# Kernel optimization log

Hardware: AMD Instinct MI355X
Metric: run time of the kernel (lower is better)

## Reference

```python
import jax, jax.numpy as jnp
import numpy as np

B, N, K, F = 1, 50000, 16, 128
EPS = 1e-5

def _bn(h, gamma, beta):
    # BatchNorm1d in training mode: per-feature-channel stats over (batch, nodes)
    mean = jnp.mean(h, axis=(0, 1), keepdims=True)
    var = jnp.var(h, axis=(0, 1), keepdims=True)
    return (h - mean) * jax.lax.rsqrt(var + EPS) * gamma + beta

def _rgcn(h, neighbors, W, b):
    # pad one zero node row, gather K neighbors per node, flatten, linear
    h_pad = jnp.pad(h, ((0, 0), (0, 1), (0, 0)))           # [B, N+1, F]
    gathered = h_pad[:, neighbors]                          # [B, N, K, F]
    flat = gathered.reshape(h.shape[0], neighbors.shape[0], -1)  # [B, N, K*F]
    return jnp.einsum('bnk,ok->bno', flat, W) + b

def setup_inputs():
    key = jax.random.key(0)
    ks = jax.random.split(key, 10)
    x = jax.random.normal(ks[0], (B, N, F), jnp.float32)
    graph = jax.random.randint(ks[1], (N, K, 2), 0, N)
    gamma1 = 1.0 + 0.1 * jax.random.normal(ks[2], (F,), jnp.float32)
    beta1 = 0.1 * jax.random.normal(ks[3], (F,), jnp.float32)
    gamma2 = 1.0 + 0.1 * jax.random.normal(ks[4], (F,), jnp.float32)
    beta2 = 0.1 * jax.random.normal(ks[5], (F,), jnp.float32)
    s = 1.0 / np.sqrt(K * F)
    W1 = jax.random.uniform(ks[6], (F, K * F), jnp.float32, -s, s)
    b1 = jax.random.uniform(ks[7], (F,), jnp.float32, -s, s)
    W2 = jax.random.uniform(ks[8], (F, K * F), jnp.float32, -s, s)
    b2 = jax.random.uniform(ks[9], (F,), jnp.float32, -s, s)
    return {"x": x, "graph": graph, "gamma1": gamma1, "beta1": beta1,
            "W1": W1, "b1": b1, "gamma2": gamma2, "beta2": beta2,
            "W2": W2, "b2": b2}

def reference(x, graph, gamma1, beta1, W1, b1, gamma2, beta2, W2, b2):
    neighbors = graph[..., 1]                               # [N, K]
    out = jax.nn.gelu(_bn(x, gamma1, beta1), approximate=False)
    out = _rgcn(out, neighbors, W1, b1)                     # [B, N, F]
    out = jax.nn.gelu(_bn(out, gamma2, beta2), approximate=False)
    out = _rgcn(out, neighbors, W2, b2)                     # [B, N, F]
    return out + x
```

## Files before the change

kernel.cpp:

```cpp
#include <hip/hip_runtime.h>


#define NN  50000
#define NB  500
#define NPB 100

typedef __bf16 v8bf __attribute__((ext_vector_type(8)));
typedef unsigned short u8s __attribute__((ext_vector_type(8)));
typedef float  v4f  __attribute__((ext_vector_type(4)));

__device__ __forceinline__ unsigned short f2bf(float f) {
  unsigned int u = __builtin_bit_cast(unsigned int, f);
  u += 0x7FFFu + ((u >> 16) & 1u);
  return (unsigned short)(u >> 16);
}
__device__ __forceinline__ float bf2f(unsigned short s) {
  unsigned int u = ((unsigned int)s) << 16;
  return __builtin_bit_cast(float, u);
}
__device__ __forceinline__ float gelu_f(float y) {
  return 0.5f * y * (1.0f + erff(y * 0.70710678118654752f));
}

__global__ void wconv_kernel(const float* __restrict__ W1, const float* __restrict__ W2,
                             unsigned short* __restrict__ Wt1, unsigned short* __restrict__ Wt2) {
  int t = blockIdx.x * 256 + threadIdx.x;
  const float* W = (t >= 32768) ? W2 : W1;
  unsigned short* Wt = (t >= 32768) ? Wt2 : Wt1;
  int r = t & 32767;
  int frag = r >> 6, lane = r & 63;
  int k4 = frag >> 3, c = frag & 7;
  int o  = c * 16 + (lane & 15);
  int kd = k4 * 32 + (lane >> 4) * 8;
  const float* src = W + o * 2048 + kd;
  unsigned short* dst = Wt + r * 8;
#pragma unroll
  for (int j = 0; j < 8; ++j) dst[j] = f2bf(src[j]);
}

__global__ void bn_stats_kernel(const float* __restrict__ x, float* __restrict__ part) {
  float s0=0,s1=0,s2=0,s3=0,q0=0,q1=0,q2=0,q3=0;
  for (int cb = blockIdx.x; cb < (NN*128/1024); cb += 256) {
    float4 v = reinterpret_cast<const float4*>(x)[cb * 256 + threadIdx.x];
    s0+=v.x; q0+=v.x*v.x; s1+=v.y; q1+=v.y*v.y;
    s2+=v.z; q2+=v.z*v.z; s3+=v.w; q3+=v.w*v.w;
  }
  __shared__ float ls[1024], lsq[1024];
  int fb = (threadIdx.x & 31) * 4;
  int sl = threadIdx.x >> 5;
  ls[sl*128+fb]   = s0; ls[sl*128+fb+1]  = s1; ls[sl*128+fb+2]  = s2; ls[sl*128+fb+3]  = s3;
  lsq[sl*128+fb]  = q0; lsq[sl*128+fb+1] = q1; lsq[sl*128+fb+2] = q2; lsq[sl*128+fb+3] = q3;
  __syncthreads();
  if (threadIdx.x < 128) {
    float S=0,Q=0;
#pragma unroll
    for (int s2i=0; s2i<8; ++s2i){ S += ls[s2i*128+threadIdx.x]; Q += lsq[s2i*128+threadIdx.x]; }
    part[blockIdx.x*256 + threadIdx.x]       = S;
    part[blockIdx.x*256 + 128 + threadIdx.x] = Q;
  }
}

__global__ __launch_bounds__(1024) void bn_reduce_kernel(
    const float* __restrict__ part, int nb,
    const float* __restrict__ gamma, const float* __restrict__ beta,
    float* __restrict__ scsh) {
  int f = threadIdx.x & 127;
  int g = threadIdx.x >> 7;
  float S = 0.f, Q = 0.f;
  for (int b = g; b < nb; b += 8) {
    S += part[b * 256 + f];
    Q += part[b * 256 + 128 + f];
  }
  __shared__ float ls[8][128], lq[8][128];
  ls[g][f] = S; lq[g][f] = Q;
  __syncthreads();
  if (threadIdx.x < 128) {
    float St = 0.f, Qt = 0.f;
#pragma unroll
    for (int i = 0; i < 8; ++i) { St += ls[i][f]; Qt += lq[i][f]; }
    float inv  = 1.0f / (float)NN;
    float mean = St * inv;
    float var  = fmaxf(Qt * inv - mean * mean, 0.0f);
    float sc   = gamma[f] * rsqrtf(var + 1e-5f);
    scsh[f]       = sc;
    scsh[128 + f] = beta[f] - mean * sc;
  }
}

__global__ void apply1_kernel(const float* __restrict__ x, const float* __restrict__ scsh,
                              unsigned short* __restrict__ h1) {
  int stride = gridDim.x * blockDim.x;
  for (int c = blockIdx.x * blockDim.x + threadIdx.x; c < NN*128/4; c += stride) {
    float4 v = reinterpret_cast<const float4*>(x)[c];
    int f = (c * 4) & 127;
    ushort4 o;
    o.x = f2bf(gelu_f(v.x * scsh[f]   + scsh[128+f]));
    o.y = f2bf(gelu_f(v.y * scsh[f+1] + scsh[128+f+1]));
    o.z = f2bf(gelu_f(v.z * scsh[f+2] + scsh[128+f+2]));
    o.w = f2bf(gelu_f(v.w * scsh[f+3] + scsh[128+f+3]));
    reinterpret_cast<ushort4*>(h1)[c] = o;
  }
}

template<int MODE>
__global__ __launch_bounds__(256, 2) void rgcn_kernel(
    const unsigned short* __restrict__ hb,
    const unsigned short* __restrict__ Wt,
    const int* __restrict__ graph,
    const float* __restrict__ scsh,
    const float* __restrict__ bias,
    const float* __restrict__ xres,
    float* __restrict__ outf,
    unsigned short* __restrict__ outb,
    float* __restrict__ part)
{
  __shared__ unsigned short bsm[16384];
  __shared__ float2 scp[128];

  const int tid  = threadIdx.x;
  const int wv   = tid >> 6;
  const int lane = tid & 63;
  const int l15  = lane & 15;
  const int lq   = lane >> 4;
  const int nb0  = blockIdx.x * NPB;
  const int nend = nb0 + NPB;

  if (MODE == 1 && tid < 128) scp[tid] = make_float2(scsh[tid], scsh[128 + tid]);

  v4f acc[2][8];
#pragma unroll
  for (int rf = 0; rf < 2; ++rf)
#pragma unroll
    for (int c = 0; c < 8; ++c) acc[rf][c] = (v4f){0.f, 0.f, 0.f, 0.f};

  const int an0 = min(nb0 + wv * 32 + l15,      nend - 1);
  const int an1 = min(nb0 + wv * 32 + 16 + l15, nend - 1);

  int idx0[16], idx1[16];
  {
    const int4* g0 = reinterpret_cast<const int4*>(graph + an0 * 32);
    const int4* g1 = reinterpret_cast<const int4*>(graph + an1 * 32);
#pragma unroll
    for (int j = 0; j < 8; ++j) {
      int4 t0 = g0[j], t1v = g1[j];
      idx0[2*j]   = min(max(t0.y,  0), NN - 1) * 128;
      idx0[2*j+1] = min(max(t0.w,  0), NN - 1) * 128;
      idx1[2*j]   = min(max(t1v.y, 0), NN - 1) * 128;
      idx1[2*j+1] = min(max(t1v.w, 0), NN - 1) * 128;
    }
  }

  u8s R0[2][4], R1[2][4];
#define LOADA(buf_, s_) {                                             \
    const unsigned short* r0 = hb + idx0[s_] + lq * 8;                \
    const unsigned short* r1 = hb + idx1[s_] + lq * 8;                \
    _Pragma("unroll")                                                 \
    for (int w4 = 0; w4 < 4; ++w4) {                                  \
      R0[buf_][w4] = *reinterpret_cast<const u8s*>(r0 + w4 * 32);     \
      R1[buf_][w4] = *reinterpret_cast<const u8s*>(r1 + w4 * 32);     \
    }                                                                 \
  }

#define STAGE(s_) {                                                           \
    const unsigned short* gsrc = Wt + (s_) * 16384 + wv * 4096 + lane * 8;    \
    unsigned short* ldst = &bsm[wv * 4096];                                   \
    _Pragma("unroll")                                                         \
    for (int i = 0; i < 8; ++i) {                                             \
      __builtin_amdgcn_global_load_lds(                                       \
        (const __attribute__((address_space(1))) void*)(gsrc + i * 512),      \
        (__attribute__((address_space(3))) void*)(ldst + i * 512),            \
        16, 0, 0);                                                            \
    }                                                                         \
  }

#define SLOT(s_) {                                                            \
    if ((s_) < 15) LOADA(((s_) + 1) & 1, (s_) + 1)                            \
    __builtin_amdgcn_sched_barrier(0);                                        \
    __builtin_amdgcn_s_setprio(1);                                            \
    {                                                                         \
      const int cur_ = (s_) & 1;                                              \
      _Pragma("unroll")                                                       \
      for (int w4 = 0; w4 < 4; ++w4) {                                        \
        v8bf a0v, a1v;                                                        \
        if constexpr (MODE == 0) {                                            \
          a0v = __builtin_bit_cast(v8bf, R0[cur_][w4]);                       \
          a1v = __builtin_bit_cast(v8bf, R1[cur_][w4]);                       \
        } else {                                                              \
          _Pragma("unroll")                                                   \
          for (int j = 0; j < 8; ++j) {                                       \
            float2 ss = scp[w4 * 32 + lq * 8 + j];                            \
            float t0 = bf2f(R0[cur_][w4][j]) * ss.x + ss.y;                   \
            float t1 = bf2f(R1[cur_][w4][j]) * ss.x + ss.y;                   \
            a0v[j] = (__bf16)(t0 * __builtin_amdgcn_rcpf(                     \
                         1.0f + __expf(-1.702f * t0)));                       \
            a1v[j] = (__bf16)(t1 * __builtin_amdgcn_rcpf(                     \
                         1.0f + __expf(-1.702f * t1)));                       \
          }                                                                   \
        }                                                                     \
        _Pragma("unroll")                                                     \
        for (int c = 0; c < 8; ++c) {                                         \
          v8bf b = *reinterpret_cast<const v8bf*>(                            \
              &bsm[(w4 * 8 + c) * 512 + lane * 8]);                           \
          acc[0][c] = __builtin_amdgcn_mfma_f32_16x16x32_bf16(                \
                        a0v, b, acc[0][c], 0, 0, 0);                          \
          acc[1][c] = __builtin_amdgcn_mfma_f32_16x16x32_bf16(                \
                        a1v, b, acc[1][c], 0, 0, 0);                          \
        }                                                                     \
      }                                                                       \
    }                                                                         \
    __builtin_amdgcn_s_setprio(0);                                            \
    __builtin_amdgcn_sched_barrier(0);                                        \
    __builtin_amdgcn_s_barrier();             \
    __builtin_amdgcn_sched_barrier(0);                                        \
    if ((s_) < 15) STAGE((s_) + 1)                                            \
    __syncthreads();                      \
  }

  STAGE(0)
  LOADA(0, 0)
  __syncthreads();

  SLOT(0)  SLOT(1)  SLOT(2)  SLOT(3)
  SLOT(4)  SLOT(5)  SLOT(6)  SLOT(7)
  SLOT(8)  SLOT(9)  SLOT(10) SLOT(11)
  SLOT(12) SLOT(13) SLOT(14) SLOT(15)
#undef SLOT
#undef LOADA
#undef STAGE

  if constexpr (MODE == 0) {
    float* lds_s = reinterpret_cast<float*>(bsm);
    float* lds_q = lds_s + 512;
#pragma unroll
    for (int c = 0; c < 8; ++c) {
      float s = 0.f, q = 0.f;
#pragma unroll
      for (int rf = 0; rf < 2; ++rf) {
#pragma unroll
        for (int j = 0; j < 4; ++j) {
          int node = nb0 + wv * 32 + rf * 16 + lq * 4 + j;
          float v  = acc[rf][c][j];
          if (node < nend) {
            s += v; q += v * v;
            outb[node * 128 + c * 16 + l15] = f2bf(v);
          }
        }
      }
      s += __shfl_xor(s, 16, 64); s += __shfl_xor(s, 32, 64);
      q += __shfl_xor(q, 16, 64); q += __shfl_xor(q, 32, 64);
      if (lq == 0) { lds_s[wv * 128 + c * 16 + l15] = s; lds_q[wv * 128 + c * 16 + l15] = q; }
    }
    __syncthreads();
    if (tid < 128) {
      float S = lds_s[tid] + lds_s[128 + tid] + lds_s[256 + tid] + lds_s[384 + tid];
      float Q = lds_q[tid] + lds_q[128 + tid] + lds_q[256 + tid] + lds_q[384 + tid];
      part[blockIdx.x * 256 + tid]       = S;
      part[blockIdx.x * 256 + 128 + tid] = Q;
    }
  } else {
#pragma unroll
    for (int c = 0; c < 8; ++c) {
      float bv = bias[c * 16 + l15];
#pragma unroll
      for (int rf = 0; rf < 2; ++rf) {
#pragma unroll
        for (int j = 0; j < 4; ++j) {
          int node = nb0 + wv * 32 + rf * 16 + lq * 4 + j;
          if (node < nend) {
            int idx = node * 128 + c * 16 + l15;
            outf[idx] = acc[rf][c][j] + bv + xres[idx];
          }
        }
      }
    }
  }
}

extern "C" void kernel_launch(void* const* d_in, const int* in_sizes, int n_in,
                              void* d_out, int out_size, void* d_ws, size_t ws_size,
                              hipStream_t stream) {
  const float* x      = (const float*)d_in[0];
  const int*   graph  = (const int*)d_in[1];
  const float* gamma1 = (const float*)d_in[2];
  const float* beta1  = (const float*)d_in[3];
  const float* W1     = (const float*)d_in[4];
  const float* gamma2 = (const float*)d_in[6];
  const float* beta2  = (const float*)d_in[7];
  const float* W2     = (const float*)d_in[8];
  const float* b2     = (const float*)d_in[9];
  float* out = (float*)d_out;

  char* ws = (char*)d_ws;
  unsigned short* h1  = (unsigned short*)(ws);
  unsigned short* t1  = (unsigned short*)(ws + 12800000);
  unsigned short* Wt1 = (unsigned short*)(ws + 25600000);
  unsigned short* Wt2 = (unsigned short*)(ws + 26124288);
  float* p1    = (float*)(ws + 26648576);
  float* p2    = (float*)(ws + 26910720);
  float* scsh1 = (float*)(ws + 27422720);
  float* scsh2 = (float*)(ws + 27423744);

  wconv_kernel<<<256, 256, 0, stream>>>(W1, W2, Wt1, Wt2);
  bn_stats_kernel<<<256, 256, 0, stream>>>(x, p1);
  bn_reduce_kernel<<<1, 1024, 0, stream>>>(p1, 256, gamma1, beta1, scsh1);
  apply1_kernel<<<2048, 256, 0, stream>>>(x, scsh1, h1);
  rgcn_kernel<0><<<NB, 256, 0, stream>>>(h1, Wt1, graph, nullptr, nullptr, nullptr,
                                         nullptr, t1, p2);
  bn_reduce_kernel<<<1, 1024, 0, stream>>>(p2, NB, gamma2, beta2, scsh2);
  rgcn_kernel<1><<<NB, 256, 0, stream>>>(t1, Wt2, graph, scsh2, b2, x,
                                         out, nullptr, nullptr);
}
```

Measured before the change: 201.2 us.

## Precompute BN2+GELU in a separate pass and coalesce t1 stores via LDS

The second BN+GELU used to be computed inside the rgcn gather loop, so every node row was recomputed once per neighbor, 16 times in total. It now runs once per element in a new elementwise apply2 kernel, and rgcn feeds the gathered bf16 rows straight into MFMA. The second-layer GELU also changes from the sigmoid approximation to the exact erf form. The first rgcn pass now stages its bf16 output tile in LDS and writes it out with coalesced 16-byte stores. The cost is an extra launch plus one more read and write pass over a 12.8 MB buffer.

```diff
diff --git a/kernel.cpp b/kernel.cpp
--- a/kernel.cpp
+++ b/kernel.cpp
@@ -102,12 +102,26 @@
   }
 }
 
+__global__ void apply2_kernel(const unsigned short* __restrict__ t1, const float* __restrict__ scsh,
+                              unsigned short* __restrict__ h2) {
+  int stride = gridDim.x * blockDim.x;
+  for (int c = blockIdx.x * blockDim.x + threadIdx.x; c < NN*128/4; c += stride) {
+    ushort4 v = reinterpret_cast<const ushort4*>(t1)[c];
+    int f = (c * 4) & 127;
+    ushort4 o;
+    o.x = f2bf(gelu_f(bf2f(v.x) * scsh[f]   + scsh[128+f]));
+    o.y = f2bf(gelu_f(bf2f(v.y) * scsh[f+1] + scsh[128+f+1]));
+    o.z = f2bf(gelu_f(bf2f(v.z) * scsh[f+2] + scsh[128+f+2]));
+    o.w = f2bf(gelu_f(bf2f(v.w) * scsh[f+3] + scsh[128+f+3]));
+    reinterpret_cast<ushort4*>(h2)[c] = o;
+  }
+}
+
 template<int MODE>
 __global__ __launch_bounds__(256, 2) void rgcn_kernel(
     const unsigned short* __restrict__ hb,
     const unsigned short* __restrict__ Wt,
     const int* __restrict__ graph,
-    const float* __restrict__ scsh,
     const float* __restrict__ bias,
     const float* __restrict__ xres,
     float* __restrict__ outf,
@@ -115,7 +129,8 @@
     float* __restrict__ part)
 {
   __shared__ unsigned short bsm[16384];
-  __shared__ float2 scp[128];
+  __shared__ float lds_s[4][128];
+  __shared__ float lds_q[4][128];
 
   const int tid  = threadIdx.x;
   const int wv   = tid >> 6;
@@ -123,9 +138,6 @@
   const int l15  = lane & 15;
   const int lq   = lane >> 4;
   const int nb0  = blockIdx.x * NPB;
-  const int nend = nb0 + NPB;
-
-  if (MODE == 1 && tid < 128) scp[tid] = make_float2(scsh[tid], scsh[128 + tid]);
 
   v4f acc[2][8];
 #pragma unroll
@@ -133,8 +145,8 @@
 #pragma unroll
     for (int c = 0; c < 8; ++c) acc[rf][c] = (v4f){0.f, 0.f, 0.f, 0.f};
 
-  const int an0 = min(nb0 + wv * 32 + l15,      nend - 1);
-  const int an1 = min(nb0 + wv * 32 + 16 + l15, nend - 1);
+  const int an0 = min(nb0 + wv * 32 + l15,      NN - 1);
+  const int an1 = min(nb0 + wv * 32 + 16 + l15, NN - 1);
 
   int idx0[16], idx1[16];
   {
@@ -150,14 +162,14 @@
     }
   }
 
-  u8s R0[2][4], R1[2][4];
+  v8bf A0[2][4], A1[2][4];
 #define LOADA(buf_, s_) {                                             \
     const unsigned short* r0 = hb + idx0[s_] + lq * 8;                \
     const unsigned short* r1 = hb + idx1[s_] + lq * 8;                \
     _Pragma("unroll")                                                 \
     for (int w4 = 0; w4 < 4; ++w4) {                                  \
-      R0[buf_][w4] = *reinterpret_cast<const u8s*>(r0 + w4 * 32);     \
-      R1[buf_][w4] = *reinterpret_cast<const u8s*>(r1 + w4 * 32);     \
+      A0[buf_][w4] = *reinterpret_cast<const v8bf*>(r0 + w4 * 32);    \
+      A1[buf_][w4] = *reinterpret_cast<const v8bf*>(r1 + w4 * 32);    \
     }                                                                 \
   }
 
@@ -174,37 +186,21 @@
   }
 
 #define SLOT(s_) {                                                            \
-    if ((s_) < 15) LOADA(((s_) + 1) & 1, (s_) + 1)                            \
+    if ((s_) < 15) LOADA(((s_) + 1) & 1, ((s_) + 1) & 15)                     \
     __builtin_amdgcn_sched_barrier(0);                                        \
     __builtin_amdgcn_s_setprio(1);                                            \
     {                                                                         \
       const int cur_ = (s_) & 1;                                              \
       _Pragma("unroll")                                                       \
       for (int w4 = 0; w4 < 4; ++w4) {                                        \
-        v8bf a0v, a1v;                                                        \
-        if constexpr (MODE == 0) {                                            \
-          a0v = __builtin_bit_cast(v8bf, R0[cur_][w4]);                       \
-          a1v = __builtin_bit_cast(v8bf, R1[cur_][w4]);                       \
-        } else {                                                              \
-          _Pragma("unroll")                                                   \
-          for (int j = 0; j < 8; ++j) {                                       \
-            float2 ss = scp[w4 * 32 + lq * 8 + j];                            \
-            float t0 = bf2f(R0[cur_][w4][j]) * ss.x + ss.y;                   \
-            float t1 = bf2f(R1[cur_][w4][j]) * ss.x + ss.y;                   \
-            a0v[j] = (__bf16)(t0 * __builtin_amdgcn_rcpf(                     \
-                         1.0f + __expf(-1.702f * t0)));                       \
-            a1v[j] = (__bf16)(t1 * __builtin_amdgcn_rcpf(                     \
-                         1.0f + __expf(-1.702f * t1)));                       \
-          }                                                                   \
-        }                                                                     \
         _Pragma("unroll")                                                     \
         for (int c = 0; c < 8; ++c) {                                         \
           v8bf b = *reinterpret_cast<const v8bf*>(                            \
               &bsm[(w4 * 8 + c) * 512 + lane * 8]);                           \
           acc[0][c] = __builtin_amdgcn_mfma_f32_16x16x32_bf16(                \
-                        a0v, b, acc[0][c], 0, 0, 0);                          \
+                        A0[cur_][w4], b, acc[0][c], 0, 0, 0);                 \
           acc[1][c] = __builtin_amdgcn_mfma_f32_16x16x32_bf16(                \
-                        a1v, b, acc[1][c], 0, 0, 0);                          \
+                        A1[cur_][w4], b, acc[1][c], 0, 0, 0);                 \
         }                                                                     \
       }                                                                       \
     }                                                                         \
@@ -212,7 +208,7 @@
     __builtin_amdgcn_sched_barrier(0);                                        \
     __builtin_amdgcn_s_barrier();             \
     __builtin_amdgcn_sched_barrier(0);                                        \
-    if ((s_) < 15) STAGE((s_) + 1)                                            \
+    if ((s_) < 15) STAGE(((s_) + 1) & 15)                                     \
     __syncthreads();                      \
   }
 
@@ -229,8 +225,6 @@
 #undef STAGE
 
   if constexpr (MODE == 0) {
-    float* lds_s = reinterpret_cast<float*>(bsm);
-    float* lds_q = lds_s + 512;
 #pragma unroll
     for (int c = 0; c < 8; ++c) {
       float s = 0.f, q = 0.f;
@@ -238,22 +232,29 @@
       for (int rf = 0; rf < 2; ++rf) {
 #pragma unroll
         for (int j = 0; j < 4; ++j) {
-          int node = nb0 + wv * 32 + rf * 16 + lq * 4 + j;
+          int lrow = wv * 32 + rf * 16 + lq * 4 + j;
           float v  = acc[rf][c][j];
-          if (node < nend) {
-            s += v; q += v * v;
-            outb[node * 128 + c * 16 + l15] = f2bf(v);
-          }
+          if (lrow < NPB) { s += v; q += v * v; }
+          bsm[lrow * 128 + c * 16 + l15] = f2bf(v);
         }
       }
       s += __shfl_xor(s, 16, 64); s += __shfl_xor(s, 32, 64);
       q += __shfl_xor(q, 16, 64); q += __shfl_xor(q, 32, 64);
-      if (lq == 0) { lds_s[wv * 128 + c * 16 + l15] = s; lds_q[wv * 128 + c * 16 + l15] = q; }
+      if (lq == 0) { lds_s[wv][c * 16 + l15] = s; lds_q[wv][c * 16 + l15] = q; }
     }
     __syncthreads();
+    unsigned short* t1b = outb + nb0 * 128;
+#pragma unroll
+    for (int i = 0; i < 7; ++i) {
+      int off = i * 2048 + tid * 8;
+      if (off < NPB * 128) {
+        *reinterpret_cast<u8s*>(t1b + off) =
+            *reinterpret_cast<const u8s*>(&bsm[off]);
+      }
+    }
     if (tid < 128) {
-      float S = lds_s[tid] + lds_s[128 + tid] + lds_s[256 + tid] + lds_s[384 + tid];
-      float Q = lds_q[tid] + lds_q[128 + tid] + lds_q[256 + tid] + lds_q[384 + tid];
+      float S = lds_s[0][tid] + lds_s[1][tid] + lds_s[2][tid] + lds_s[3][tid];
+      float Q = lds_q[0][tid] + lds_q[1][tid] + lds_q[2][tid] + lds_q[3][tid];
       part[blockIdx.x * 256 + tid]       = S;
       part[blockIdx.x * 256 + 128 + tid] = Q;
     }
@@ -266,7 +267,7 @@
 #pragma unroll
         for (int j = 0; j < 4; ++j) {
           int node = nb0 + wv * 32 + rf * 16 + lq * 4 + j;
-          if (node < nend) {
+          if (node < nb0 + NPB) {
             int idx = node * 128 + c * 16 + l15;
             outf[idx] = acc[rf][c][j] + bv + xres[idx];
           }
@@ -304,9 +305,10 @@
   bn_stats_kernel<<<256, 256, 0, stream>>>(x, p1);
   bn_reduce_kernel<<<1, 1024, 0, stream>>>(p1, 256, gamma1, beta1, scsh1);
   apply1_kernel<<<2048, 256, 0, stream>>>(x, scsh1, h1);
-  rgcn_kernel<0><<<NB, 256, 0, stream>>>(h1, Wt1, graph, nullptr, nullptr, nullptr,
+  rgcn_kernel<0><<<NB, 256, 0, stream>>>(h1, Wt1, graph, nullptr, nullptr,
                                          nullptr, t1, p2);
   bn_reduce_kernel<<<1, 1024, 0, stream>>>(p2, NB, gamma2, beta2, scsh2);
-  rgcn_kernel<1><<<NB, 256, 0, stream>>>(t1, Wt2, graph, scsh2, b2, x,
+  apply2_kernel<<<2048, 256, 0, stream>>>(t1, scsh2, h1);
+  rgcn_kernel<1><<<NB, 256, 0, stream>>>(h1, Wt2, graph, b2, x,
                                          out, nullptr, nullptr);
 }
```

New measurement: 202.1 us. About the same (+0.5%).
